# Kernel optimization log

Measured on AMD Instinct MI355X. Metric: run time of the kernel, lower is better.

Reference implementation:

```python
import jax, jax.numpy as jnp
import numpy as np

N = 65536          # nodes
G = 512            # graphs (num_segments for scatter-mean)
NB = 10            # number_of_basis
MAXR = 10.0        # max_radius
NODE_DIM = 64      # 48 z-embed + 16 mol-embed scalars
MUL = 16           # multiplicity of each output irrep l=0..3
WNUM = NODE_DIM * 4 * MUL  # tp weight numel = 4096
MID = 32           # middle_layer_size

_trapz = getattr(np, 'trapezoid', np.trapz)

def _silu_norm():
    # e3nn normalize2mom constant for silu: 1/sqrt(E_{z~N(0,1)}[silu(z)^2]) ~= 1.679
    z = np.linspace(-12.0, 12.0, 200001)
    pdf = np.exp(-0.5 * z * z) / np.sqrt(2.0 * np.pi)
    s = z / (1.0 + np.exp(-z))
    return float(_trapz(s * s * pdf, z) ** -0.5)

SILU_C = _silu_norm()

def soft_unit_step(x):
    pos = x > 0
    return jnp.where(pos, jnp.exp(-1.0 / jnp.where(pos, x, 1.0)), 0.0)

def soft_one_hot_smooth_finite(x):
    # e3nn soft_one_hot_linspace(basis='smooth_finite', cutoff=True)
    values = jnp.linspace(0.0, MAXR, NB + 2)[1:-1]
    step = MAXR / (NB + 1)
    diff = (x[:, None] - values) / step
    c = 1.14136 * float(np.exp(2.0))
    return c * soft_unit_step(diff + 1.0) * soft_unit_step(1.0 - diff)

def spherical_harmonics_lmax3(vec):
    # e3nn convention, normalize=True, normalization='component' (each l scaled by sqrt(2l+1))
    u = vec / jnp.linalg.norm(vec, axis=-1, keepdims=True)
    x, y, z = u[..., 0], u[..., 1], u[..., 2]
    s3 = np.sqrt(3.0)
    y2, x2z2 = y * y, x * x + z * z
    sh0 = jnp.ones_like(x)[..., None]
    s20 = s3 * x * z; s21 = s3 * x * y; s22 = y2 - 0.5 * x2z2
    s23 = s3 * y * z; s24 = 0.5 * s3 * (z * z - x * x)
    s30 = np.sqrt(5.0 / 6.0) * (s20 * z + s24 * x)
    s31 = np.sqrt(5.0) * s20 * y
    s32 = np.sqrt(3.0 / 8.0) * (4.0 * y2 - x2z2) * x
    s33 = 0.5 * y * (2.0 * y2 - 3.0 * x2z2)
    s34 = np.sqrt(3.0 / 8.0) * z * (4.0 * y2 - x2z2)
    s35 = np.sqrt(5.0) * s24 * y
    s36 = np.sqrt(5.0 / 6.0) * (s24 * z - s20 * x)
    sh1 = np.sqrt(3.0) * jnp.stack([x, y, z], -1)
    sh2 = np.sqrt(5.0) * jnp.stack([s20, s21, s22, s23, s24], -1)
    sh3 = np.sqrt(7.0) * jnp.stack([s30, s31, s32, s33, s34, s35, s36], -1)
    return (sh0, sh1, sh2, sh3)

def setup_inputs() -> dict:
    key = jax.random.key(0)
    ks = jax.random.split(key, 8)
    pos = 3.0 * jax.random.normal(ks[0], (N, 3), jnp.float32)
    x = jax.random.randint(ks[1], (N,), 0, 100)
    mol_id = jax.random.randint(ks[2], (N,), 0, 3)
    batch = jnp.sort(jax.random.randint(ks[3], (N,), 0, G))
    emb_z = jax.random.normal(ks[4], (100, 48), jnp.float32)
    emb_mol = jax.random.normal(ks[5], (3, 16), jnp.float32)
    W1 = jax.random.normal(ks[6], (NB, MID), jnp.float32)
    W2 = jax.random.normal(ks[7], (MID, WNUM), jnp.float32)
    return {'pos': pos, 'x': x, 'mol_id': mol_id, 'batch': batch,
            'emb_z': emb_z, 'emb_mol': emb_mol, 'W1': W1, 'W2': W2}

def reference(pos, x, mol_id, batch, emb_z, emb_mol, W1, W2):
    feat = jnp.concatenate([emb_z[x], emb_mol[mol_id]], axis=-1)        # [N, 64]
    length = jnp.linalg.norm(pos, axis=1)
    basis = soft_one_hot_smooth_finite(length) * np.sqrt(float(NB))     # [N, 10]
    # e3nn FullyConnectedNet([10, 32, 4096], silu): weight / sqrt(fan_in), normalized silu
    h = SILU_C * jax.nn.silu(basis @ (W1 / np.sqrt(float(NB))))         # [N, 32]
    w = h @ (W2 / np.sqrt(float(MID)))                                  # [N, 4096]
    # path weight sqrt((2l+1)/64) times w3j(0,l,l)=I/sqrt(2l+1) -> net factor 1/sqrt(64)
    w = w.reshape(-1, 4, NODE_DIM, MUL)
    xw = jnp.einsum('eu,eluw->elw', feat, w) / np.sqrt(float(NODE_DIM))  # [N, 4, 16]
    shs = spherical_harmonics_lmax3(pos)
    blocks = [(xw[:, l, :, None] * shs[l][:, None, :]).reshape(-1, MUL * (2 * l + 1)) for l in range(4)]
    value = jnp.concatenate(blocks, axis=-1)                            # [N, 256]
    sums = jax.ops.segment_sum(value, batch, num_segments=G)
    counts = jax.ops.segment_sum(jnp.ones((value.shape[0], 1), value.dtype), batch, num_segments=G)
    return sums / jnp.maximum(counts, 1.0)                              # scatter-mean [G, 256]
```

## Files before the change

### kernel.cpp

```cpp
#include <hip/hip_runtime.h>
#include <math.h>

#define N_NODES 65536
#define G_SEG   512
#define NE      256

#define NB_E  257
#define NB_S  3
#define NB_P0 (N_NODES / 256)
#define NB_ALL (NB_E + NB_S + NB_P0)

#define CH 4

#define A_ELEMS (257 * 100 * 64)
#define B_ELEMS (257 * 3 * 64)

__global__ __launch_bounds__(256) void build_AB(
    const float* __restrict__ emb_z, const float* __restrict__ emb_mol,
    const float* __restrict__ W2, const float* __restrict__ W1,
    const int* __restrict__ batch,
    const float* __restrict__ pos, const int* __restrict__ xz,
    const int* __restrict__ mol,
    float* __restrict__ A, float* __restrict__ B,
    int* __restrict__ seg, float4* __restrict__ aux, float silu_c)
{
    __shared__ float w2h[64 * 64];
    __shared__ float ezs[100 * 48];
    __shared__ float emol[48];
    __shared__ float hsrow[32];

    const int b = blockIdx.x;
    const int t = threadIdx.x;

    if (b < NB_E) {
        const int e = b;

        for (int p = t; p < 4800; p += 256) ezs[p] = emb_z[p];
        if (t < 48) emol[t] = emb_mol[t];
        if (t < 32) {
            const int m = t;
            const float L = (float)e * (10.f / (float)NE);
            const float c = 8.4335412f;
            float p = 0.f;
#pragma unroll
            for (int k = 0; k < 10; ++k) {
                const float a  = 1.1f * L - (float)k;
                const float bb = (float)(k + 2) - 1.1f * L;
                const float bas = (a > 0.f && bb > 0.f) ? c * __expf(-2.f / (a * bb)) : 0.f;
                p = fmaf(bas, W1[k * 32 + m], p);
            }
            hsrow[m] = silu_c * p / (1.f + __expf(-p));
        }
        __syncthreads();

        {
            const int j  = t & 63;
            const int l  = j >> 4, wi = j & 15;
            const int u0 = (t >> 6) * 16;
            const float scale = 0.02209708691207961f;
            float acc[16];
#pragma unroll
            for (int q = 0; q < 16; ++q) acc[q] = 0.f;
            const float* wbase = W2 + l * 1024 + wi + u0 * 16;
            for (int m = 0; m < 32; ++m) {
                const float h = hsrow[m];
                const float* wp = wbase + m * 4096;
#pragma unroll
                for (int q = 0; q < 16; ++q)
                    acc[q] = fmaf(h, wp[q * 16], acc[q]);
            }
#pragma unroll
            for (int q = 0; q < 16; ++q)
                w2h[(u0 + q) * 64 + j] = acc[q] * scale;
        }
        __syncthreads();

        {
            const int j  = t & 63;
            const int zg = t >> 6;
            float accz[25];
#pragma unroll
            for (int zi = 0; zi < 25; ++zi) accz[zi] = 0.f;
            for (int ut = 0; ut < 48; ut += 8) {
                float wr[8];
#pragma unroll
                for (int q = 0; q < 8; ++q) wr[q] = w2h[(ut + q) * 64 + j];
#pragma unroll
                for (int zi = 0; zi < 25; ++zi) {
                    const int z = zg + 4 * zi;
#pragma unroll
                    for (int q = 0; q < 8; ++q)
                        accz[zi] = fmaf(ezs[z * 48 + ut + q], wr[q], accz[zi]);
                }
            }
#pragma unroll
            for (int zi = 0; zi < 25; ++zi)
                A[((e * 100 + zg + 4 * zi) << 6) + j] = accz[zi];

            if (t < 192) {
                const int mo = t >> 6;
                float s = 0.f;
#pragma unroll
                for (int q = 0; q < 16; ++q)
                    s = fmaf(emol[mo * 16 + q], w2h[(48 + q) * 64 + j], s);
                B[((e * 3 + mo) << 6) + j] = s;
            }
        }
    } else if (b < NB_E + NB_S) {
        const int g = (b - NB_E) * 256 + t;
        if (g > G_SEG) return;
        int lo = 0, hi = N_NODES;
        while (lo < hi) {
            const int mid = (lo + hi) >> 1;
            if (batch[mid] < g) lo = mid + 1; else hi = mid;
        }
        seg[g] = lo;
    } else {
        const int i = (b - NB_E - NB_S) * 256 + t;
        const float px = pos[3 * i], py = pos[3 * i + 1], pz = pos[3 * i + 2];
        const int z  = xz[i];
        const int mo = mol[i];
        const float Lsq = px * px + py * py + pz * pz;
        const float rinv = __builtin_amdgcn_rsqf(Lsq);
        const float L = Lsq * rinv;
        const float tt = fminf(L * ((float)NE / 10.0f), 255.999f);
        const int e = (int)tt;
        const int fr15 = min((int)((tt - (float)e) * 32768.f), 32767);
        float4 a;
        a.x = px * rinv; a.y = py * rinv; a.z = pz * rinv;
        a.w = __uint_as_float(((unsigned)e << 24) | ((unsigned)z << 17) |
                              ((unsigned)mo << 15) | (unsigned)fr15);
        aux[i] = a;
    }
}

__global__ __launch_bounds__(256) void seg_xw(
    const float4* __restrict__ aux, const int* __restrict__ seg,
    const float* __restrict__ A, const float* __restrict__ B,
    float* __restrict__ partials)
{
    __shared__ float red[4 * 257];

    const int g = blockIdx.x >> 2;
    const int c = blockIdx.x & 3;
    const int s0 = seg[g], s1 = seg[g + 1];
    const int cnt = s1 - s0;
    const int q0 = s0 + (cnt * c) / CH;
    const int q1 = s0 + (cnt * (c + 1)) / CH;

    const int l    = __builtin_amdgcn_readfirstlane(threadIdx.x >> 6);
    const int lane = threadIdx.x & 63;
    const int ns   = lane >> 4;
    const int wi   = lane & 15;
    const int jj   = l * 16 + wi;

    float acc[7];
#pragma unroll
    for (int k = 0; k < 7; ++k) acc[k] = 0.f;

    const int niter = (q1 - q0 + 3) >> 2;

    float4 aN = make_float4(0.f, 0.f, 1.f, __uint_as_float(0u));
    float a0N = 0.f, a1N = 0.f, b0N = 0.f, b1N = 0.f;
    if (niter > 0) {
        const int ic = min(q0 + ns, q1 - 1);
        aN = aux[ic];
        const unsigned cd = __float_as_uint(aN.w);
        const float* Ar = A + (((cd >> 24) * 100 + ((cd >> 17) & 127u)) << 6) + jj;
        const float* Br = B + (((cd >> 24) * 3 + ((cd >> 15) & 3u)) << 6) + jj;
        a0N = Ar[0]; a1N = Ar[6400]; b0N = Br[0]; b1N = Br[192];
    }

    for (int it = 0; it < niter; ++it) {
        const float4 a = aN;
        const float f0 = a0N + b0N, f1 = a1N + b1N;
        const unsigned code = __float_as_uint(a.w);
        const int i = q0 + it * 4 + ns;
        const bool valid = (i < q1);

        if (it + 1 < niter) {
            const int ic = min(q0 + (it + 1) * 4 + ns, q1 - 1);
            aN = aux[ic];
            const unsigned cn = __float_as_uint(aN.w);
            const float* Ar = A + (((cn >> 24) * 100 + ((cn >> 17) & 127u)) << 6) + jj;
            const float* Br = B + (((cn >> 24) * 3 + ((cn >> 15) & 3u)) << 6) + jj;
            a0N = Ar[0]; a1N = Ar[6400]; b0N = Br[0]; b1N = Br[192];
        }

        const float fr = (float)(code & 32767u) * 3.0517578125e-5f;
        float xwv = fmaf(fr, f1 - f0, f0);
        xwv = valid ? xwv : 0.f;

        const float ux = a.x, uy = a.y, uz = a.z;
        const float s3 = 1.7320508075688772f, s5 = 2.2360679774997896f, s7 = 2.6457513110645907f;

        if (l == 0) {
            acc[0] += xwv;
        } else if (l == 1) {
            acc[0] = fmaf(xwv, s3 * ux, acc[0]);
            acc[1] = fmaf(xwv, s3 * uy, acc[1]);
            acc[2] = fmaf(xwv, s3 * uz, acc[2]);
        } else if (l == 2) {
            const float y2 = uy * uy, x2z2 = ux * ux + uz * uz;
            const float s20 = s3 * ux * uz;
            const float s21 = s3 * ux * uy;
            const float s22 = y2 - 0.5f * x2z2;
            const float s23 = s3 * uy * uz;
            const float s24 = 0.5f * s3 * (uz * uz - ux * ux);
            const float xs = xwv * s5;
            acc[0] = fmaf(xs, s20, acc[0]);
            acc[1] = fmaf(xs, s21, acc[1]);
            acc[2] = fmaf(xs, s22, acc[2]);
            acc[3] = fmaf(xs, s23, acc[3]);
            acc[4] = fmaf(xs, s24, acc[4]);
        } else {
            const float y2 = uy * uy, x2z2 = ux * ux + uz * uz;
            const float s20 = s3 * ux * uz;
            const float s24 = 0.5f * s3 * (uz * uz - ux * ux);
            const float c56 = 0.9128709291752769f;
            const float c38 = 0.6123724356957945f;
            const float r4 = 4.f * y2 - x2z2;
            const float s30 = c56 * (s20 * uz + s24 * ux);
            const float s31 = s5 * s20 * uy;
            const float s32 = c38 * r4 * ux;
            const float s33 = 0.5f * uy * (2.f * y2 - 3.f * x2z2);
            const float s34 = c38 * uz * r4;
            const float s35 = s5 * s24 * uy;
            const float s36 = c56 * (s24 * uz - s20 * ux);
            const float xs = xwv * s7;
            acc[0] = fmaf(xs, s30, acc[0]);
            acc[1] = fmaf(xs, s31, acc[1]);
            acc[2] = fmaf(xs, s32, acc[2]);
            acc[3] = fmaf(xs, s33, acc[3]);
            acc[4] = fmaf(xs, s34, acc[4]);
            acc[5] = fmaf(xs, s35, acc[5]);
            acc[6] = fmaf(xs, s36, acc[6]);
        }
    }

    const int nl = 2 * l + 1;
    const int off = (l == 0 ? 0 : (l == 1 ? 16 : (l == 2 ? 64 : 144)));
    const int base = off + wi * nl;
#pragma unroll
    for (int k = 0; k < 7; ++k)
        if (k < nl) red[ns * 257 + base + k] = acc[k];
    __syncthreads();

    if (threadIdx.x < 256) {
        float s = 0.f;
#pragma unroll
        for (int ww = 0; ww < 4; ++ww) s += red[ww * 257 + threadIdx.x];
        partials[blockIdx.x * 256 + threadIdx.x] = s;
    }
}

__global__ __launch_bounds__(256) void reduce(
    const float* __restrict__ partials, const int* __restrict__ seg,
    float* __restrict__ out)
{
    const int g = blockIdx.x;
    const int t = threadIdx.x;
    const int cnt = seg[g + 1] - seg[g];
    float s = 0.f;
#pragma unroll
    for (int c = 0; c < CH; ++c)
        s += partials[(g * CH + c) * 256 + t];
    out[g * 256 + t] = s / (float)max(cnt, 1);
}

static double silu_c_host()
{
    const int n = 200001;
    const double h = 24.0 / 200000.0;
    double sum = 0.0, prev = 0.0;
    for (int i = 0; i < n; ++i) {
        const double z = -12.0 + h * (double)i;
        const double pdf = exp(-0.5 * z * z) * 0.3989422804014327;
        const double s = z / (1.0 + exp(-z));
        const double f = s * s * pdf;
        if (i) sum += prev + f;
        prev = f;
    }
    sum *= 0.5 * h;
    return 1.0 / sqrt(sum);
}

extern "C" void kernel_launch(void* const* d_in, const int* in_sizes, int n_in,
                              void* d_out, int out_size, void* d_ws, size_t ws_size,
                              hipStream_t stream)
{
    const float* pos     = (const float*)d_in[0];
    const int*   xz      = (const int*)d_in[1];
    const int*   mol     = (const int*)d_in[2];
    const int*   batch   = (const int*)d_in[3];
    const float* emb_z   = (const float*)d_in[4];
    const float* emb_mol = (const float*)d_in[5];
    const float* W1      = (const float*)d_in[6];
    const float* W2      = (const float*)d_in[7];
    float* out = (float*)d_out;

    float*  Abuf  = (float*)d_ws;
    float*  Bbuf  = Abuf + A_ELEMS;
    int*    seg   = (int*)(Bbuf + B_ELEMS);
    float4* aux   = (float4*)((float*)seg + 1024);
    float*  parts = (float*)aux + 4 * N_NODES;

    static const float SILU_C_F = (float)silu_c_host();

    build_AB<<<NB_ALL, 256, 0, stream>>>(emb_z, emb_mol, W2, W1, batch,
                                         pos, xz, mol, Abuf, Bbuf, seg, aux, SILU_C_F);
    seg_xw<<<G_SEG * CH, 256, 0, stream>>>(aux, seg, Abuf, Bbuf, parts);
    reduce<<<G_SEG, 256, 0, stream>>>(parts, seg, out);
}
```

Before: 39.61 us.

## Reassociate table build via emb_z×W2 precompute and fuse segment reduction

The per-bin table build is reassociated. A table Q = emb_z·W2 (per z, per hidden unit) and Qm are computed once, and each A entry then becomes a 32-term dot of the hidden row with Q. This replaces the per-bin 64×64 W2h product plus the 100×48 contraction, spreading the table work across many more, lighter blocks in a new middle kernel. The segment kernel now uses 512-thread blocks covering a whole graph in two halves and writes the mean directly, which removes the partials buffer and the separate reduce kernel. The cost is one extra launch and a global round-trip for Q and hs.

```diff
diff --git a/kernel.cpp b/kernel.cpp
--- a/kernel.cpp
+++ b/kernel.cpp
@@ -5,109 +5,94 @@
 #define G_SEG   512
 #define NE      256
 
-#define NB_E  257
+#define NB_HS 33
+#define NB_Q  128
+#define NB_QM 32
 #define NB_S  3
 #define NB_P0 (N_NODES / 256)
-#define NB_ALL (NB_E + NB_S + NB_P0)
-
-#define CH 4
-
-#define A_ELEMS (257 * 100 * 64)
-#define B_ELEMS (257 * 3 * 64)
-
-__global__ __launch_bounds__(256) void build_AB(
+#define NB_K1 (NB_HS + NB_Q + NB_QM + NB_S + NB_P0)
+
+#define NB_A  1700
+#define NB_B2 257
+#define NB_K2 (NB_A + NB_B2)
+
+#define A_ELEMS  (257 * 100 * 64)
+#define B_ELEMS  (257 * 3 * 64)
+#define Q_ELEMS  (100 * 32 * 64)
+#define QM_ELEMS (3 * 32 * 64)
+#define HS_ELEMS (257 * 32)
+
+__global__ __launch_bounds__(256) void prep1(
     const float* __restrict__ emb_z, const float* __restrict__ emb_mol,
     const float* __restrict__ W2, const float* __restrict__ W1,
     const int* __restrict__ batch,
     const float* __restrict__ pos, const int* __restrict__ xz,
     const int* __restrict__ mol,
-    float* __restrict__ A, float* __restrict__ B,
+    float* __restrict__ Q, float* __restrict__ Qm, float* __restrict__ hs,
     int* __restrict__ seg, float4* __restrict__ aux, float silu_c)
 {
-    __shared__ float w2h[64 * 64];
-    __shared__ float ezs[100 * 48];
-    __shared__ float emol[48];
-    __shared__ float hsrow[32];
+    __shared__ float w2s[64 * 49];
+    __shared__ float ezq[1200];
 
     const int b = blockIdx.x;
     const int t = threadIdx.x;
 
-    if (b < NB_E) {
-        const int e = b;
-
-        for (int p = t; p < 4800; p += 256) ezs[p] = emb_z[p];
-        if (t < 48) emol[t] = emb_mol[t];
-        if (t < 32) {
-            const int m = t;
-            const float L = (float)e * (10.f / (float)NE);
-            const float c = 8.4335412f;
-            float p = 0.f;
-#pragma unroll
-            for (int k = 0; k < 10; ++k) {
-                const float a  = 1.1f * L - (float)k;
-                const float bb = (float)(k + 2) - 1.1f * L;
-                const float bas = (a > 0.f && bb > 0.f) ? c * __expf(-2.f / (a * bb)) : 0.f;
-                p = fmaf(bas, W1[k * 32 + m], p);
+    if (b < NB_HS) {
+        const int tid = b * 256 + t;
+        if (tid >= HS_ELEMS) return;
+        const int e = tid >> 5, m = tid & 31;
+        const float L = (float)e * (10.f / (float)NE);
+        const float c = 8.4335412f;
+        float p = 0.f;
+#pragma unroll
+        for (int k = 0; k < 10; ++k) {
+            const float a  = 1.1f * L - (float)k;
+            const float bb = (float)(k + 2) - 1.1f * L;
+            const float bas = (a > 0.f && bb > 0.f) ? c * __expf(-2.f / (a * bb)) : 0.f;
+            p = fmaf(bas, W1[k * 32 + m], p);
+        }
+        const float scale = 0.02209708691207961f;
+        hs[tid] = scale * silu_c * p / (1.f + __expf(-p));
+    } else if (b < NB_HS + NB_Q) {
+        const int q  = b - NB_HS;
+        const int m  = q >> 2;
+        const int zq = q & 3;
+        for (int p = t; p < 3072; p += 256) {
+            const int l = p / 768, r = p - l * 768;
+            w2s[((l * 16) + (r & 15)) * 49 + (r >> 4)] = W2[m * 4096 + l * 1024 + r];
+        }
+        for (int p = t; p < 1200; p += 256) ezq[p] = emb_z[zq * 1200 + p];
+        __syncthreads();
+
+        const int zg = t >> 6, cc = t & 63;
+#pragma unroll
+        for (int zi = 0; zi < 7; ++zi) {
+            const int zl = zg + 4 * zi;
+            if (zl < 25) {
+                float a0 = 0.f, a1 = 0.f, a2 = 0.f, a3 = 0.f;
+#pragma unroll
+                for (int u = 0; u < 48; u += 4) {
+                    a0 = fmaf(ezq[zl * 48 + u + 0], w2s[cc * 49 + u + 0], a0);
+                    a1 = fmaf(ezq[zl * 48 + u + 1], w2s[cc * 49 + u + 1], a1);
+                    a2 = fmaf(ezq[zl * 48 + u + 2], w2s[cc * 49 + u + 2], a2);
+                    a3 = fmaf(ezq[zl * 48 + u + 3], w2s[cc * 49 + u + 3], a3);
+                }
+                Q[(((zq * 25 + zl) * 32 + m) << 6) + cc] = (a0 + a1) + (a2 + a3);
             }
-            hsrow[m] = silu_c * p / (1.f + __expf(-p));
-        }
-        __syncthreads();
-
-        {
-            const int j  = t & 63;
-            const int l  = j >> 4, wi = j & 15;
-            const int u0 = (t >> 6) * 16;
-            const float scale = 0.02209708691207961f;
-            float acc[16];
-#pragma unroll
-            for (int q = 0; q < 16; ++q) acc[q] = 0.f;
-            const float* wbase = W2 + l * 1024 + wi + u0 * 16;
-            for (int m = 0; m < 32; ++m) {
-                const float h = hsrow[m];
-                const float* wp = wbase + m * 4096;
-#pragma unroll
-                for (int q = 0; q < 16; ++q)
-                    acc[q] = fmaf(h, wp[q * 16], acc[q]);
-            }
-#pragma unroll
-            for (int q = 0; q < 16; ++q)
-                w2h[(u0 + q) * 64 + j] = acc[q] * scale;
-        }
-        __syncthreads();
-
-        {
-            const int j  = t & 63;
-            const int zg = t >> 6;
-            float accz[25];
-#pragma unroll
-            for (int zi = 0; zi < 25; ++zi) accz[zi] = 0.f;
-            for (int ut = 0; ut < 48; ut += 8) {
-                float wr[8];
-#pragma unroll
-                for (int q = 0; q < 8; ++q) wr[q] = w2h[(ut + q) * 64 + j];
-#pragma unroll
-                for (int zi = 0; zi < 25; ++zi) {
-                    const int z = zg + 4 * zi;
-#pragma unroll
-                    for (int q = 0; q < 8; ++q)
-                        accz[zi] = fmaf(ezs[z * 48 + ut + q], wr[q], accz[zi]);
-                }
-            }
-#pragma unroll
-            for (int zi = 0; zi < 25; ++zi)
-                A[((e * 100 + zg + 4 * zi) << 6) + j] = accz[zi];
-
-            if (t < 192) {
-                const int mo = t >> 6;
-                float s = 0.f;
-#pragma unroll
-                for (int q = 0; q < 16; ++q)
-                    s = fmaf(emol[mo * 16 + q], w2h[(48 + q) * 64 + j], s);
-                B[((e * 3 + mo) << 6) + j] = s;
-            }
-        }
-    } else if (b < NB_E + NB_S) {
-        const int g = (b - NB_E) * 256 + t;
+        }
+    } else if (b < NB_HS + NB_Q + NB_QM) {
+        const int m = b - (NB_HS + NB_Q);
+        if (t < 192) {
+            const int mo = t >> 6, j = t & 63;
+            const float* wp = W2 + m * 4096 + (j >> 4) * 1024 + 768 + (j & 15);
+            float acc = 0.f;
+#pragma unroll
+            for (int v = 0; v < 16; ++v)
+                acc = fmaf(emb_mol[mo * 16 + v], wp[v * 16], acc);
+            Qm[((mo * 32 + m) << 6) + j] = acc;
+        }
+    } else if (b < NB_HS + NB_Q + NB_QM + NB_S) {
+        const int g = (b - NB_HS - NB_Q - NB_QM) * 256 + t;
         if (g > G_SEG) return;
         int lo = 0, hi = N_NODES;
         while (lo < hi) {
@@ -116,7 +101,7 @@
         }
         seg[g] = lo;
     } else {
-        const int i = (b - NB_E - NB_S) * 256 + t;
+        const int i = (b - NB_HS - NB_Q - NB_QM - NB_S) * 256 + t;
         const float px = pos[3 * i], py = pos[3 * i + 1], pz = pos[3 * i + 2];
         const int z  = xz[i];
         const int mo = mol[i];
@@ -134,25 +119,78 @@
     }
 }
 
-__global__ __launch_bounds__(256) void seg_xw(
+__global__ __launch_bounds__(256) void build_AB2(
+    const float* __restrict__ Q, const float* __restrict__ Qm,
+    const float* __restrict__ hs,
+    float* __restrict__ A, float* __restrict__ B)
+{
+    const int b = blockIdx.x;
+    const int t = threadIdx.x;
+    const int j = t & 63;
+    const int er = __builtin_amdgcn_readfirstlane(t >> 6);
+
+    if (b < NB_A) {
+        const int et = b / 100;
+        const int z  = b - et * 100;
+        float Qr[32];
+        const float* Qp = Q + ((z * 32) << 6) + j;
+#pragma unroll
+        for (int m = 0; m < 32; ++m) Qr[m] = Qp[m << 6];
+
+        const int e0 = et * 16;
+#pragma unroll
+        for (int p4 = 0; p4 < 4; ++p4) {
+            const int e = e0 + er + 4 * p4;
+            if (e < 257) {
+                const float* hp = hs + e * 32;
+                float a0 = 0.f, a1 = 0.f, a2 = 0.f, a3 = 0.f;
+#pragma unroll
+                for (int m = 0; m < 32; m += 4) {
+                    a0 = fmaf(hp[m + 0], Qr[m + 0], a0);
+                    a1 = fmaf(hp[m + 1], Qr[m + 1], a1);
+                    a2 = fmaf(hp[m + 2], Qr[m + 2], a2);
+                    a3 = fmaf(hp[m + 3], Qr[m + 3], a3);
+                }
+                A[((e * 100 + z) << 6) + j] = (a0 + a1) + (a2 + a3);
+            }
+        }
+    } else {
+        const int e  = b - NB_A;
+        const int mo = t >> 6;
+        if (mo < 3) {
+            const float* Qp = Qm + ((mo * 32) << 6) + j;
+            const float* hp = hs + e * 32;
+            float acc = 0.f;
+#pragma unroll
+            for (int m = 0; m < 32; ++m)
+                acc = fmaf(hp[m], Qp[m << 6], acc);
+            B[((e * 3 + mo) << 6) + j] = acc;
+        }
+    }
+}
+
+__global__ __launch_bounds__(512) void seg_mean(
     const float4* __restrict__ aux, const int* __restrict__ seg,
     const float* __restrict__ A, const float* __restrict__ B,
-    float* __restrict__ partials)
-{
-    __shared__ float red[4 * 257];
-
-    const int g = blockIdx.x >> 2;
-    const int c = blockIdx.x & 3;
+    float* __restrict__ out)
+{
+    __shared__ float red[8 * 257];
+
+    const int g  = blockIdx.x;
     const int s0 = seg[g], s1 = seg[g + 1];
     const int cnt = s1 - s0;
-    const int q0 = s0 + (cnt * c) / CH;
-    const int q1 = s0 + (cnt * (c + 1)) / CH;
-
-    const int l    = __builtin_amdgcn_readfirstlane(threadIdx.x >> 6);
+
+    const int w8   = __builtin_amdgcn_readfirstlane(threadIdx.x >> 6);
+    const int l    = w8 & 3;
+    const int hf   = w8 >> 2;
     const int lane = threadIdx.x & 63;
     const int ns   = lane >> 4;
     const int wi   = lane & 15;
     const int jj   = l * 16 + wi;
+
+    const int mid = s0 + ((cnt + 1) >> 1);
+    const int q0 = hf ? mid : s0;
+    const int q1 = hf ? s1 : mid;
 
     float acc[7];
 #pragma unroll
@@ -243,29 +281,15 @@
     const int base = off + wi * nl;
 #pragma unroll
     for (int k = 0; k < 7; ++k)
-        if (k < nl) red[ns * 257 + base + k] = acc[k];
+        if (k < nl) red[(hf * 4 + ns) * 257 + base + k] = acc[k];
     __syncthreads();
 
     if (threadIdx.x < 256) {
         float s = 0.f;
 #pragma unroll
-        for (int ww = 0; ww < 4; ++ww) s += red[ww * 257 + threadIdx.x];
-        partials[blockIdx.x * 256 + threadIdx.x] = s;
-    }
-}
-
-__global__ __launch_bounds__(256) void reduce(
-    const float* __restrict__ partials, const int* __restrict__ seg,
-    float* __restrict__ out)
-{
-    const int g = blockIdx.x;
-    const int t = threadIdx.x;
-    const int cnt = seg[g + 1] - seg[g];
-    float s = 0.f;
-#pragma unroll
-    for (int c = 0; c < CH; ++c)
-        s += partials[(g * CH + c) * 256 + t];
-    out[g * 256 + t] = s / (float)max(cnt, 1);
+        for (int ww = 0; ww < 8; ++ww) s += red[ww * 257 + threadIdx.x];
+        out[g * 256 + threadIdx.x] = s / (float)max(cnt, 1);
+    }
 }
 
 static double silu_c_host()
@@ -299,16 +323,18 @@
     const float* W2      = (const float*)d_in[7];
     float* out = (float*)d_out;
 
-    float*  Abuf  = (float*)d_ws;
-    float*  Bbuf  = Abuf + A_ELEMS;
-    int*    seg   = (int*)(Bbuf + B_ELEMS);
-    float4* aux   = (float4*)((float*)seg + 1024);
-    float*  parts = (float*)aux + 4 * N_NODES;
+    float4* aux  = (float4*)d_ws;
+    float*  Abuf = (float*)d_ws + 4 * N_NODES;
+    float*  Bbuf = Abuf + A_ELEMS;
+    float*  Qbuf = Bbuf + B_ELEMS;
+    float*  Qmb  = Qbuf + Q_ELEMS;
+    float*  hsb  = Qmb + QM_ELEMS;
+    int*    seg  = (int*)(hsb + HS_ELEMS);
 
     static const float SILU_C_F = (float)silu_c_host();
 
-    build_AB<<<NB_ALL, 256, 0, stream>>>(emb_z, emb_mol, W2, W1, batch,
-                                         pos, xz, mol, Abuf, Bbuf, seg, aux, SILU_C_F);
-    seg_xw<<<G_SEG * CH, 256, 0, stream>>>(aux, seg, Abuf, Bbuf, parts);
-    reduce<<<G_SEG, 256, 0, stream>>>(parts, seg, out);
-}
+    prep1<<<NB_K1, 256, 0, stream>>>(emb_z, emb_mol, W2, W1, batch,
+                                     pos, xz, mol, Qbuf, Qmb, hsb, seg, aux, SILU_C_F);
+    build_AB2<<<NB_K2, 256, 0, stream>>>(Qbuf, Qmb, hsb, Abuf, Bbuf);
+    seg_mean<<<G_SEG, 512, 0, stream>>>(aux, seg, Abuf, Bbuf, out);
+}
```

Result: no change. 39.52 us (-0.2%).
